# Performance work log

Measured on AMD Instinct MI355X. Metric: run time of the kernel, lower is better.

Reference implementation:

```python
import jax, jax.numpy as jnp
import numpy as np

N_NODES = 100000
N_EDGES = 1600000
D_IN = 64
D_OUT = 64


def setup_inputs() -> dict:
    key = jax.random.key(0)
    k1, k2, k3, k4 = jax.random.split(key, 4)
    x = jax.random.normal(k1, (N_NODES, D_IN), dtype=jnp.float32)
    W = jax.random.normal(k2, (D_OUT, D_IN), dtype=jnp.float32) * 0.1
    b = jax.random.normal(k3, (D_OUT,), dtype=jnp.float32) * 0.1
    edge_index = jax.random.randint(k4, (2, N_EDGES), 0, N_NODES, dtype=jnp.int64 if jax.config.jax_enable_x64 else jnp.int32)
    return {"x": x, "W": W, "b": b, "edge_index": edge_index}


def reference(x, W, b, edge_index):
    N = x.shape[0]
    # add self loops
    loop = jnp.arange(N, dtype=edge_index.dtype)
    src = jnp.concatenate([edge_index[0], loop])  # row: source nodes
    dst = jnp.concatenate([edge_index[1], loop])  # col: target nodes
    E = src.shape[0]

    # linear transform
    h = x @ W.T + b  # [N, D_OUT]

    # degree over source (row) indices, as in the original message()
    ones = jnp.ones((E,), dtype=h.dtype)
    deg = jax.ops.segment_sum(ones, src, num_segments=N)  # [N]
    deg_inv_sqrt = jnp.where(deg > 0, jax.lax.rsqrt(jnp.maximum(deg, 1.0)), 0.0)
    norm = deg_inv_sqrt[src] * deg_inv_sqrt[dst]  # [E]

    # gather-scale messages, then scatter-mean into targets
    msg = norm[:, None] * h[src]  # [E, D_OUT]
    agg_sum = jax.ops.segment_sum(msg, dst, num_segments=N)  # [N, D_OUT]
    cnt = jax.ops.segment_sum(ones, dst, num_segments=N)  # [N]
    out = agg_sum / jnp.maximum(cnt, 1.0)[:, None]
    return out
```

## Files before the change

### kernel.cpp

```cpp
#include <hip/hip_runtime.h>
#include <hip/hip_fp16.h>

#define N_D 64
#define PB_D 6
#define PSZ_D 64
#define CAP_D 1536
#define SCAP  2048
#define PB_S 7
#define PSZ_S 128
#define CAP_S 3072

__global__ __launch_bounds__(1024) void scatter_kernel(const int* __restrict__ src,
                                                       const int* __restrict__ dst,
                                                       int* __restrict__ cursorD,
                                                       int* __restrict__ cursorS,
                                                       unsigned* __restrict__ epart,
                                                       unsigned char* __restrict__ spart,
                                                       int E, int PD, int PS) {
    extern __shared__ int sh[];
    int* hD = sh;
    int* hS = sh + PD;
    int* bD = sh + PD + PS;
    int* bS = sh + 2 * PD + PS;
    int t = threadIdx.x;
    for (int i = t; i < PD + PS; i += 1024) sh[i] = 0;
    __syncthreads();
    const int4* src4 = (const int4*)src;
    const int4* dst4 = (const int4*)dst;
    int E4 = E >> 2;
    int per = (E4 + gridDim.x - 1) / gridDim.x;
    int beg = blockIdx.x * per, end = min(E4, beg + per);
    bool tailblk = (blockIdx.x == 0);
    for (int e = beg + t; e < end; e += 1024) {
        int4 d = dst4[e];
        int4 s = src4[e];
        atomicAdd(&hD[d.x >> PB_D], 1);
        atomicAdd(&hD[d.y >> PB_D], 1);
        atomicAdd(&hD[d.z >> PB_D], 1);
        atomicAdd(&hD[d.w >> PB_D], 1);
        atomicAdd(&hS[s.x >> PB_S], 1);
        atomicAdd(&hS[s.y >> PB_S], 1);
        atomicAdd(&hS[s.z >> PB_S], 1);
        atomicAdd(&hS[s.w >> PB_S], 1);
    }
    if (tailblk) {
        for (int e = (E4 << 2) + t; e < E; e += 1024) {
            atomicAdd(&hD[dst[e] >> PB_D], 1);
            atomicAdd(&hS[src[e] >> PB_S], 1);
        }
    }
    __syncthreads();
    for (int p = t; p < PD; p += 1024) {
        int hd = hD[p];
        if (hd) {
            int r = atomicAdd(&cursorD[p], hd);
            if (r > CAP_D - hd) r = max(CAP_D - hd, 0);
            bD[p] = r;
        }
        hD[p] = 0;
    }
    for (int p = t; p < PS; p += 1024) {
        int hs_ = hS[p];
        if (hs_) {
            int r = atomicAdd(&cursorS[p], hs_);
            if (r > CAP_S - hs_) r = max(CAP_S - hs_, 0);
            bS[p] = r;
        }
        hS[p] = 0;
    }
    __syncthreads();
    for (int e = beg + t; e < end; e += 1024) {
        int4 dv = dst4[e];
        int4 sv = src4[e];
        int ds_[4] = {dv.x, dv.y, dv.z, dv.w};
        int ss_[4] = {sv.x, sv.y, sv.z, sv.w};
#pragma unroll
        for (int k = 0; k < 4; k++) {
            int d = ds_[k], s0 = ss_[k];
            int pd = d >> PB_D, ps = s0 >> PB_S;
            int od = atomicAdd(&hD[pd], 1);
            epart[(size_t)pd * CAP_D + bD[pd] + od] =
                ((unsigned)s0 << PB_D) | (unsigned)(d & (PSZ_D - 1));
            int os = atomicAdd(&hS[ps], 1);
            spart[(size_t)ps * CAP_S + bS[ps] + os] = (unsigned char)(s0 & (PSZ_S - 1));
        }
    }
    if (tailblk) {
        for (int e = (E4 << 2) + t; e < E; e += 1024) {
            int d = dst[e], s0 = src[e];
            int pd = d >> PB_D, ps = s0 >> PB_S;
            int od = atomicAdd(&hD[pd], 1);
            epart[(size_t)pd * CAP_D + bD[pd] + od] =
                ((unsigned)s0 << PB_D) | (unsigned)(d & (PSZ_D - 1));
            int os = atomicAdd(&hS[ps], 1);
            spart[(size_t)ps * CAP_S + bS[ps] + os] = (unsigned char)(s0 & (PSZ_S - 1));
        }
    }
}

#define LROWS 128
__global__ __launch_bounds__(256) void linear_kernel(const float* __restrict__ x,
                                                     const float* __restrict__ W,
                                                     const float* __restrict__ b,
                                                     const unsigned char* __restrict__ spart,
                                                     const int* __restrict__ cursorS,
                                                     float* __restrict__ dis,
                                                     __half* __restrict__ hs, int N) {
    __shared__ float xs[LROWS][N_D + 1];
    __shared__ float Wt[N_D][N_D + 4];
    __shared__ float bs[N_D];
    __shared__ int ohist[PSZ_S];
    __shared__ float disS[PSZ_S];

    int tid = threadIdx.x;
    int p = blockIdx.x;
    if (p == 0 && tid < 32) ((int*)hs)[(size_t)N * 32 + tid] = 0;
    if (tid < PSZ_S) ohist[tid] = 0;
    for (int i = tid; i < N_D * N_D; i += 256) {
        int o = i >> 6, k = i & 63;
        Wt[k][o] = W[i];
    }
    if (tid < N_D) bs[tid] = b[tid];
    __syncthreads();

    {
        size_t sbase = (size_t)p * CAP_S;
        int len = min(cursorS[p], CAP_S);
        const unsigned* sp4 = (const unsigned*)(spart + sbase);
        int n4 = len >> 2;
        for (int i = tid; i < n4; i += 256) {
            unsigned v = sp4[i];
            atomicAdd(&ohist[v & 127], 1);
            atomicAdd(&ohist[(v >> 8) & 127], 1);
            atomicAdd(&ohist[(v >> 16) & 127], 1);
            atomicAdd(&ohist[(v >> 24) & 127], 1);
        }
        for (int i = (n4 << 2) + tid; i < len; i += 256)
            atomicAdd(&ohist[spart[sbase + i]], 1);
    }

    int row0 = p * LROWS;
    const float4* x4 = (const float4*)(x + (size_t)row0 * N_D);
    const int n4x = LROWS * N_D / 4;
    if (row0 + LROWS <= N) {
        for (int i = tid; i < n4x; i += 256) {
            float4 v = x4[i];
            int r = i >> 4, kq = (i & 15) << 2;
            xs[r][kq] = v.x; xs[r][kq + 1] = v.y; xs[r][kq + 2] = v.z; xs[r][kq + 3] = v.w;
        }
    } else {
        for (int i = tid; i < n4x; i += 256) {
            int r = i >> 4, kq = (i & 15) << 2;
            float4 v = make_float4(0.f, 0.f, 0.f, 0.f);
            if (row0 + r < N) v = x4[i];
            xs[r][kq] = v.x; xs[r][kq + 1] = v.y; xs[r][kq + 2] = v.z; xs[r][kq + 3] = v.w;
        }
    }
    __syncthreads();

    if (tid < PSZ_S) {
        float dv = rsqrtf((float)(ohist[tid] + 1));
        disS[tid] = dv;
        int node = row0 + tid;
        if (node < N) dis[node] = dv;
    }
    __syncthreads();

    int tc = tid >> 5;
    int tr = tid & 31;
    float acc[4][8];
#pragma unroll
    for (int j = 0; j < 4; j++)
#pragma unroll
        for (int i = 0; i < 8; i++) acc[j][i] = 0.f;

#pragma unroll 4
    for (int k = 0; k < N_D; k++) {
        float4 w0 = *(const float4*)&Wt[k][tc * 8];
        float4 w1 = *(const float4*)&Wt[k][tc * 8 + 4];
        float wv[8] = {w0.x, w0.y, w0.z, w0.w, w1.x, w1.y, w1.z, w1.w};
        float xv[4];
#pragma unroll
        for (int j = 0; j < 4; j++) xv[j] = xs[tr + 32 * j][k];
#pragma unroll
        for (int j = 0; j < 4; j++)
#pragma unroll
            for (int i = 0; i < 8; i++) acc[j][i] += xv[j] * wv[i];
    }

#pragma unroll
    for (int j = 0; j < 4; j++) {
        int row = row0 + tr + 32 * j;
        if (row < N) {
            float dr = disS[tr + 32 * j];
            union { __half h[8]; int4 v; } u;
#pragma unroll
            for (int i = 0; i < 8; i++)
                u.h[i] = __float2half_rn((acc[j][i] + bs[tc * 8 + i]) * dr);
            *(int4*)(hs + (size_t)row * N_D + tc * 8) = u.v;
        }
    }
}

__device__ __forceinline__ void acc8(int4 v, float* a) {
    union { int i; __half2 h; } u;
    float2 f;
    u.i = v.x; f = __half22float2(u.h); a[0] += f.x; a[1] += f.y;
    u.i = v.y; f = __half22float2(u.h); a[2] += f.x; a[3] += f.y;
    u.i = v.z; f = __half22float2(u.h); a[4] += f.x; a[5] += f.y;
    u.i = v.w; f = __half22float2(u.h); a[6] += f.x; a[7] += f.y;
}

__global__ __launch_bounds__(256) void gather_part_kernel(const unsigned* __restrict__ epart,
                                                          const int* __restrict__ cursorD,
                                                          const __half* __restrict__ hs,
                                                          const float* __restrict__ dis,
                                                          float* __restrict__ out, int N) {
    __shared__ unsigned raw[CAP_D];
    __shared__ int sorted[SCAP];
    __shared__ int hist[PSZ_D];
    __shared__ int rs[PSZ_D];
    __shared__ int cur[PSZ_D];
    int p = blockIdx.x, t = threadIdx.x;
    if (t < PSZ_D) hist[t] = 0;
    __syncthreads();
    size_t base = (size_t)p * CAP_D;
    int num = min(cursorD[p], CAP_D);
    {
        const uint4* ep4 = (const uint4*)(epart + base);
        int n4 = num >> 2;
        for (int i4 = t; i4 < n4; i4 += 256) {
            uint4 v = ep4[i4];
            ((uint4*)raw)[i4] = v;
            atomicAdd(&hist[v.x & (PSZ_D - 1)], 1);
            atomicAdd(&hist[v.y & (PSZ_D - 1)], 1);
            atomicAdd(&hist[v.z & (PSZ_D - 1)], 1);
            atomicAdd(&hist[v.w & (PSZ_D - 1)], 1);
        }
        for (int i = (n4 << 2) + t; i < num; i += 256) {
            unsigned e = epart[base + i];
            raw[i] = e;
            atomicAdd(&hist[e & (PSZ_D - 1)], 1);
        }
    }
    __syncthreads();
    int v = 0;
    if (t < PSZ_D) { v = (hist[t] + 8) & ~7; rs[t] = v; }
    __syncthreads();
    for (int off = 1; off < PSZ_D; off <<= 1) {
        int x = 0;
        if (t < PSZ_D && t >= off) x = rs[t - off];
        __syncthreads();
        if (t < PSZ_D) rs[t] += x;
        __syncthreads();
    }
    if (t < PSZ_D) { int ex = rs[t] - v; rs[t] = ex; cur[t] = ex; }
    __syncthreads();
    if (t < PSZ_D) {
        int cnt = hist[t];
        int pb = rs[t] + cnt;
        int pad = ((cnt + 8) & ~7) - cnt;
        sorted[pb] = ((p << PB_D) + t) << 7;
        const int ZERO_OFF = N << 7;
        for (int k = 1; k < pad; k++) sorted[pb + k] = ZERO_OFF;
    }
    for (int i = t; i < num; i += 256) {
        unsigned e = raw[i];
        int pos = atomicAdd(&cur[e & (PSZ_D - 1)], 1);
        sorted[pos] = (int)((e & ~(unsigned)(PSZ_D - 1)) << 1);
    }
    __syncthreads();
    int w = t >> 6, lane = t & 63;
    int g = lane & 7, q = lane >> 3;
    int qb = q << 4;
    const char* hbase = (const char*)hs;
    for (int r = w * 16; r < w * 16 + 16; r++) {
        int node = (p << PB_D) + r;
        if (node >= N) break;
        int jb = rs[r];
        int cnt = hist[r];
        int cntP = (cnt + 8) & ~7;
        float a[8];
#pragma unroll
        for (int i = 0; i < 8; i++) a[i] = 0.f;
        int j = 0;
        for (; j + 16 <= cntP; j += 16) {
            int o0 = sorted[jb + j + g];
            int o1 = sorted[jb + j + 8 + g];
            int4 v0 = *(const int4*)(hbase + (size_t)(unsigned)(o0 + qb));
            int4 v1 = *(const int4*)(hbase + (size_t)(unsigned)(o1 + qb));
            acc8(v0, a);
            acc8(v1, a);
        }
        for (; j < cntP; j += 8) {
            int o = sorted[jb + j + g];
            int4 v0 = *(const int4*)(hbase + (size_t)(unsigned)(o + qb));
            acc8(v0, a);
        }
#pragma unroll
        for (int m = 1; m <= 4; m <<= 1) {
#pragma unroll
            for (int i = 0; i < 8; i++) a[i] += __shfl_xor(a[i], m, 64);
        }
        float scale = dis[node] / (float)(cnt + 1);
        if (g == 0) {
            float4 w0 = make_float4(a[0] * scale, a[1] * scale, a[2] * scale, a[3] * scale);
            float4 w1 = make_float4(a[4] * scale, a[5] * scale, a[6] * scale, a[7] * scale);
            float4* op = (float4*)(out + ((size_t)node << 6) + (q << 3));
            op[0] = w0;
            op[1] = w1;
        }
    }
}

extern "C" void kernel_launch(void* const* d_in, const int* in_sizes, int n_in,
                              void* d_out, int out_size, void* d_ws, size_t ws_size,
                              hipStream_t stream) {
    const float* x = (const float*)d_in[0];
    const float* W = (const float*)d_in[1];
    const float* b = (const float*)d_in[2];
    const int* edge_index = (const int*)d_in[3];

    const int N = in_sizes[0] / N_D;
    const int E = in_sizes[3] / 2;
    const int* src = edge_index;
    const int* dst = edge_index + E;
    float* out = (float*)d_out;

    const int PD = (N + PSZ_D - 1) / PSZ_D;
    const int PS = (N + PSZ_S - 1) / PSZ_S;

    char* ws = (char*)d_ws;
    size_t off = 0;
    __half* hs = (__half*)(ws + off);         off += ((size_t)(N + 1) * N_D * sizeof(__half) + 15) & ~15ull;
    float* dis = (float*)(ws + off);          off += (size_t)N * sizeof(float);
    unsigned* epart = (unsigned*)(ws + off);  off += (size_t)PD * CAP_D * sizeof(unsigned);
    unsigned char* spart = (unsigned char*)(ws + off); off += (size_t)PS * CAP_S;
    int* cursorD = (int*)(ws + off);          off += (size_t)PD * sizeof(int);
    int* cursorS = (int*)(ws + off);          off += (size_t)PS * sizeof(int);
    (void)ws_size;

    size_t lds_scat = 2u * (PD + PS) * sizeof(int);

    hipMemsetAsync(cursorD, 0, (size_t)(PD + PS) * sizeof(int), stream);

    scatter_kernel<<<256, 1024, lds_scat, stream>>>(src, dst, cursorD, cursorS,
                                                    epart, spart, E, PD, PS);
    linear_kernel<<<PS, 256, 0, stream>>>(x, W, b, spart, cursorS, dis, hs, N);
    gather_part_kernel<<<PD, 256, 0, stream>>>(epart, cursorD, hs, dis, out, N);
}
```

Before: 187.1 us.

## Flatten per-node gather into continuous group stream with eight-deep load batching

Rewrites the gather phase so each wavefront walks a flat sequence of 8-edge groups spanning its 16 nodes, using a shared group-to-node map to flush accumulators at node boundaries. This lets eight independent 16-byte loads be issued back to back across node boundaries, increasing memory-level parallelism instead of draining per node. It also replaces the shared-memory Hillis-Steele scan with a wavefront shuffle scan, which removes a series of block barriers, and caches dis values in LDS. The cost is an extra LDS lookup and a divergent flush branch per group.

```diff
diff --git a/kernel.cpp b/kernel.cpp
--- a/kernel.cpp
+++ b/kernel.cpp
@@ -6,6 +6,7 @@
 #define PSZ_D 64
 #define CAP_D 1536
 #define SCAP  2048
+#define GCAP  (SCAP / 8)
 #define PB_S 7
 #define PSZ_S 128
 #define CAP_S 3072
@@ -221,6 +222,8 @@
     __shared__ int hist[PSZ_D];
     __shared__ int rs[PSZ_D];
     __shared__ int cur[PSZ_D];
+    __shared__ short gnode[GCAP + 8];
+    __shared__ float disL[PSZ_D];
     int p = blockIdx.x, t = threadIdx.x;
     if (t < PSZ_D) hist[t] = 0;
     __syncthreads();
@@ -244,72 +247,103 @@
         }
     }
     __syncthreads();
-    int v = 0;
-    if (t < PSZ_D) { v = (hist[t] + 8) & ~7; rs[t] = v; }
-    __syncthreads();
-    for (int off = 1; off < PSZ_D; off <<= 1) {
-        int x = 0;
-        if (t < PSZ_D && t >= off) x = rs[t - off];
-        __syncthreads();
-        if (t < PSZ_D) rs[t] += x;
-        __syncthreads();
-    }
-    if (t < PSZ_D) { int ex = rs[t] - v; rs[t] = ex; cur[t] = ex; }
-    __syncthreads();
     if (t < PSZ_D) {
+        int v = (hist[t] + 8) & ~7;
+        int s = v;
+#pragma unroll
+        for (int off = 1; off < PSZ_D; off <<= 1) {
+            int n = __shfl_up(s, off, 64);
+            if (t >= off) s += n;
+        }
+        int ex = s - v;
+        rs[t] = ex;
+        cur[t] = ex;
         int cnt = hist[t];
-        int pb = rs[t] + cnt;
+        int node = (p << PB_D) + t;
+        int pb = ex + cnt;
         int pad = ((cnt + 8) & ~7) - cnt;
-        sorted[pb] = ((p << PB_D) + t) << 7;
         const int ZERO_OFF = N << 7;
+        sorted[pb] = (node < N) ? (node << 7) : ZERO_OFF;
         for (int k = 1; k < pad; k++) sorted[pb + k] = ZERO_OFF;
-    }
+        int g0 = ex >> 3, g1 = (ex + cnt + pad) >> 3;
+        for (int G = g0; G < g1; ++G) gnode[G] = (short)t;
+        if (t == PSZ_D - 1) gnode[g1] = -1;
+        disL[t] = (node < N) ? dis[node] : 0.f;
+    }
+    __syncthreads();
     for (int i = t; i < num; i += 256) {
         unsigned e = raw[i];
         int pos = atomicAdd(&cur[e & (PSZ_D - 1)], 1);
         sorted[pos] = (int)((e & ~(unsigned)(PSZ_D - 1)) << 1);
     }
     __syncthreads();
+
     int w = t >> 6, lane = t & 63;
     int g = lane & 7, q = lane >> 3;
     int qb = q << 4;
     const char* hbase = (const char*)hs;
-    for (int r = w * 16; r < w * 16 + 16; r++) {
-        int node = (p << PB_D) + r;
-        if (node >= N) break;
-        int jb = rs[r];
-        int cnt = hist[r];
-        int cntP = (cnt + 8) & ~7;
-        float a[8];
-#pragma unroll
-        for (int i = 0; i < 8; i++) a[i] = 0.f;
-        int j = 0;
-        for (; j + 16 <= cntP; j += 16) {
-            int o0 = sorted[jb + j + g];
-            int o1 = sorted[jb + j + 8 + g];
-            int4 v0 = *(const int4*)(hbase + (size_t)(unsigned)(o0 + qb));
-            int4 v1 = *(const int4*)(hbase + (size_t)(unsigned)(o1 + qb));
-            acc8(v0, a);
-            acc8(v1, a);
-        }
-        for (; j < cntP; j += 8) {
-            int o = sorted[jb + j + g];
-            int4 v0 = *(const int4*)(hbase + (size_t)(unsigned)(o + qb));
-            acc8(v0, a);
-        }
-#pragma unroll
-        for (int m = 1; m <= 4; m <<= 1) {
-#pragma unroll
-            for (int i = 0; i < 8; i++) a[i] += __shfl_xor(a[i], m, 64);
-        }
-        float scale = dis[node] / (float)(cnt + 1);
-        if (g == 0) {
-            float4 w0 = make_float4(a[0] * scale, a[1] * scale, a[2] * scale, a[3] * scale);
-            float4 w1 = make_float4(a[4] * scale, a[5] * scale, a[6] * scale, a[7] * scale);
-            float4* op = (float4*)(out + ((size_t)node << 6) + (q << 3));
-            op[0] = w0;
-            op[1] = w1;
-        }
+    int r0 = w * 16;
+    int rlast = r0 + 15;
+    int G = rs[r0] >> 3;
+    int gend = (rs[rlast] + ((hist[rlast] + 8) & ~7)) >> 3;
+    int r = r0;
+    float a[8];
+#pragma unroll
+    for (int i = 0; i < 8; i++) a[i] = 0.f;
+
+    auto proc = [&](int4 v, int Gi) {
+        acc8(v, a);
+        int nr = gnode[Gi + 1];
+        if (nr != r) {
+#pragma unroll
+            for (int m = 1; m <= 4; m <<= 1)
+#pragma unroll
+                for (int i = 0; i < 8; i++) a[i] += __shfl_xor(a[i], m, 64);
+            int node = (p << PB_D) + r;
+            float scale = disL[r] / (float)(hist[r] + 1);
+            if (g == 0 && node < N) {
+                float4* op = (float4*)(out + ((size_t)node << 6) + (q << 3));
+                op[0] = make_float4(a[0] * scale, a[1] * scale, a[2] * scale, a[3] * scale);
+                op[1] = make_float4(a[4] * scale, a[5] * scale, a[6] * scale, a[7] * scale);
+            }
+#pragma unroll
+            for (int i = 0; i < 8; i++) a[i] = 0.f;
+            r = nr;
+        }
+    };
+
+    while (G + 8 <= gend) {
+        int o0 = sorted[(G + 0) * 8 + g] + qb;
+        int o1 = sorted[(G + 1) * 8 + g] + qb;
+        int o2 = sorted[(G + 2) * 8 + g] + qb;
+        int o3 = sorted[(G + 3) * 8 + g] + qb;
+        int o4 = sorted[(G + 4) * 8 + g] + qb;
+        int o5 = sorted[(G + 5) * 8 + g] + qb;
+        int o6 = sorted[(G + 6) * 8 + g] + qb;
+        int o7 = sorted[(G + 7) * 8 + g] + qb;
+        int4 v0 = *(const int4*)(hbase + (size_t)(unsigned)o0);
+        int4 v1 = *(const int4*)(hbase + (size_t)(unsigned)o1);
+        int4 v2 = *(const int4*)(hbase + (size_t)(unsigned)o2);
+        int4 v3 = *(const int4*)(hbase + (size_t)(unsigned)o3);
+        int4 v4 = *(const int4*)(hbase + (size_t)(unsigned)o4);
+        int4 v5 = *(const int4*)(hbase + (size_t)(unsigned)o5);
+        int4 v6 = *(const int4*)(hbase + (size_t)(unsigned)o6);
+        int4 v7 = *(const int4*)(hbase + (size_t)(unsigned)o7);
+        proc(v0, G + 0);
+        proc(v1, G + 1);
+        proc(v2, G + 2);
+        proc(v3, G + 3);
+        proc(v4, G + 4);
+        proc(v5, G + 5);
+        proc(v6, G + 6);
+        proc(v7, G + 7);
+        G += 8;
+    }
+    while (G < gend) {
+        int o = sorted[G * 8 + g] + qb;
+        int4 v = *(const int4*)(hbase + (size_t)(unsigned)o);
+        proc(v, G);
+        ++G;
     }
 }
 
```

Result: no change. 185.5 us, median of 2 (-0.9%).
